# Performance work log

Hardware: AMD Instinct MI355X
Metric: run time of the kernel (lower is better)

## Reference

```python
import jax, jax.numpy as jnp
import numpy as np


def setup_inputs() -> dict:
    key = jax.random.key(0)
    k1, k2 = jax.random.split(key)
    x1 = jax.random.normal(k1, (8192, 256), dtype=jnp.float32)
    x2 = jax.random.normal(k2, (8192, 256), dtype=jnp.float32)
    return {"x1": x1, "x2": x2}


def reference(x1, x2):
    # Euclidean distance matrix, equivalent to torch.cdist(x1, x2, p=2.0).
    # GEMM-based expansion: ||a-b||^2 = ||a||^2 + ||b||^2 - 2 a.b
    sq1 = jnp.sum(x1 * x1, axis=-1, keepdims=True)          # [N, 1]
    sq2 = jnp.sum(x2 * x2, axis=-1, keepdims=True)          # [M, 1]
    cross = jnp.einsum('nd,md->nm', x1, x2)                 # [N, M]
    d2 = sq1 + sq2.T - 2.0 * cross
    d2 = jnp.maximum(d2, 0.0)  # guard tiny negatives from cancellation
    return jnp.sqrt(d2)
```

## Files before the change

### kernel.cpp

```cpp
#include <hip/hip_runtime.h>


typedef __bf16 v8bf __attribute__((ext_vector_type(8)));
typedef float v4f __attribute__((ext_vector_type(4)));

#define NROWS 8192
#define KDIM  256
#define TILE  128
#define BK    64

typedef const __attribute__((address_space(1))) ushort* gas_ushort_p;
typedef __attribute__((address_space(3))) ushort* las_ushort_p;

__device__ __forceinline__ void async_load16(const ushort* g, ushort* l) {
    __builtin_amdgcn_global_load_lds((gas_ushort_p)g, (las_ushort_p)l, 16, 0, 0);
}

__device__ __forceinline__ ushort f2bf_rne(float f) {
    union { float f; unsigned u; } a; a.f = f;
    unsigned u = a.u + 0x7fffu + ((a.u >> 16) & 1u);
    return (ushort)(u >> 16);
}

__global__ __launch_bounds__(256) void cvt_norm_kernel(
    const float* __restrict__ x, ushort* __restrict__ xb, float* __restrict__ sq) {
    const int wave = threadIdx.x >> 6;
    const int lane = threadIdx.x & 63;
    const int row  = blockIdx.x * 4 + wave;
    const float4 v = ((const float4*)(x + (size_t)row * KDIM))[lane];
    float s = v.x * v.x + v.y * v.y + v.z * v.z + v.w * v.w;
#pragma unroll
    for (int off = 32; off; off >>= 1) s += __shfl_down(s, off);
    if (lane == 0) sq[row] = s;
    ushort4 o;
    o.x = f2bf_rne(v.x); o.y = f2bf_rne(v.y);
    o.z = f2bf_rne(v.z); o.w = f2bf_rne(v.w);
    ((ushort4*)(xb + (size_t)row * KDIM))[lane] = o;
}

__global__ __launch_bounds__(256) void cdist_mfma_kernel(
    const ushort* __restrict__ A,
    const ushort* __restrict__ B,
    const float* __restrict__ sq1,
    const float* __restrict__ sq2,
    float* __restrict__ out) {
    __shared__ ushort As[TILE * BK];
    __shared__ ushort Bs[TILE * BK];

    const int bm = blockIdx.x, bn = blockIdx.y;
    const int tid  = threadIdx.x;
    const int wave = tid >> 6;
    const int lane = tid & 63;
    const int wr = wave >> 1;
    const int wc = wave & 1;

    const int lrow = lane >> 3;
    const int lk   = (lane & 7) * 8;

    v4f acc[4][4];
#pragma unroll
    for (int i = 0; i < 4; ++i)
#pragma unroll
        for (int j = 0; j < 4; ++j) acc[i][j] = (v4f){0.f, 0.f, 0.f, 0.f};

    const int half = lane >> 4;
    const int mrow = lane & 15;

    for (int kt = 0; kt < KDIM; kt += BK) {
        __syncthreads();
#pragma unroll
        for (int c = 0; c < 4; ++c) {
            const int rbase = wave * 32 + c * 8;
            const ushort* ga =
                A + (size_t)(bm * TILE + rbase + lrow) * KDIM + kt + lk;
            const ushort* gb =
                B + (size_t)(bn * TILE + rbase + lrow) * KDIM + kt + lk;
            async_load16(ga, &As[rbase * BK]);
            async_load16(gb, &Bs[rbase * BK]);
        }
        __syncthreads();
#pragma unroll
        for (int kk = 0; kk < BK; kk += 32) {
            v8bf a[4], b[4];
#pragma unroll
            for (int i = 0; i < 4; ++i) {
                a[i] = *(const v8bf*)&As[(wr * 64 + i * 16 + mrow) * BK + kk + half * 8];
                b[i] = *(const v8bf*)&Bs[(wc * 64 + i * 16 + mrow) * BK + kk + half * 8];
            }
#pragma unroll
            for (int i = 0; i < 4; ++i)
#pragma unroll
                for (int j = 0; j < 4; ++j)
                    acc[i][j] = __builtin_amdgcn_mfma_f32_16x16x32_bf16(
                        a[i], b[j], acc[i][j], 0, 0, 0);
        }
    }

    const int m0 = bm * TILE + wr * 64;
    const int n0 = bn * TILE + wc * 64;
#pragma unroll
    for (int j = 0; j < 4; ++j) {
        const int col = n0 + j * 16 + mrow;
        const float s2 = sq2[col];
#pragma unroll
        for (int i = 0; i < 4; ++i) {
#pragma unroll
            for (int r = 0; r < 4; ++r) {
                const int row = m0 + i * 16 + half * 4 + r;
                const float d2 = sq1[row] + s2 - 2.0f * acc[i][j][r];
                out[(size_t)row * NROWS + col] = sqrtf(fmaxf(d2, 0.0f));
            }
        }
    }
}

extern "C" void kernel_launch(void* const* d_in, const int* in_sizes, int n_in,
                              void* d_out, int out_size, void* d_ws, size_t ws_size,
                              hipStream_t stream) {
    const float* x1 = (const float*)d_in[0];
    const float* x2 = (const float*)d_in[1];
    float* out = (float*)d_out;

    ushort* Ab = (ushort*)d_ws;
    ushort* Bb = Ab + (size_t)NROWS * KDIM;
    float* sq1 = (float*)(Bb + (size_t)NROWS * KDIM);
    float* sq2 = sq1 + NROWS;

    cvt_norm_kernel<<<NROWS / 4, 256, 0, stream>>>(x1, Ab, sq1);
    cvt_norm_kernel<<<NROWS / 4, 256, 0, stream>>>(x2, Bb, sq2);

    dim3 grid(NROWS / TILE, NROWS / TILE);
    cdist_mfma_kernel<<<grid, 256, 0, stream>>>(Ab, Bb, sq1, sq2, out);
}
```

Measured before the change: 355.0 us.

## Drop LDS staging for register-direct double-buffered loads with XCD-aware tile mapping

The GEMM kernel no longer stages tiles through shared memory with barriers. Each wave now loads its MFMA operands straight from global memory into registers, double-buffering across the eight k-steps. Blocks are remapped so that tiles sharing rows or columns land on the same XCD, which improves L2 reuse. Output uses nontemporal stores, and the two conversion launches are merged into one. The risks are redundant global loads across waves in place of shared LDS reuse, and higher register pressure.

Measured after the change: 382.3 us. +7.7%, slower.

```diff
diff --git a/kernel.cpp b/kernel.cpp
--- a/kernel.cpp
+++ b/kernel.cpp
@@ -6,15 +6,6 @@
 
 #define NROWS 8192
 #define KDIM  256
-#define TILE  128
-#define BK    64
-
-typedef const __attribute__((address_space(1))) ushort* gas_ushort_p;
-typedef __attribute__((address_space(3))) ushort* las_ushort_p;
-
-__device__ __forceinline__ void async_load16(const ushort* g, ushort* l) {
-    __builtin_amdgcn_global_load_lds((gas_ushort_p)g, (las_ushort_p)l, 16, 0, 0);
-}
 
 __device__ __forceinline__ ushort f2bf_rne(float f) {
     union { float f; unsigned u; } a; a.f = f;
@@ -23,10 +14,18 @@
 }
 
 __global__ __launch_bounds__(256) void cvt_norm_kernel(
-    const float* __restrict__ x, ushort* __restrict__ xb, float* __restrict__ sq) {
+    const float* __restrict__ x1, const float* __restrict__ x2,
+    ushort* __restrict__ xb1, ushort* __restrict__ xb2,
+    float* __restrict__ sq1, float* __restrict__ sq2) {
+    const int half2 = NROWS / 4;
+    const float* x = (blockIdx.x < half2) ? x1 : x2;
+    ushort* xb     = (blockIdx.x < half2) ? xb1 : xb2;
+    float* sq      = (blockIdx.x < half2) ? sq1 : sq2;
+    const int bb   = (blockIdx.x < half2) ? blockIdx.x : blockIdx.x - half2;
+
     const int wave = threadIdx.x >> 6;
     const int lane = threadIdx.x & 63;
-    const int row  = blockIdx.x * 4 + wave;
+    const int row  = bb * 4 + wave;
     const float4 v = ((const float4*)(x + (size_t)row * KDIM))[lane];
     float s = v.x * v.x + v.y * v.y + v.z * v.z + v.w * v.w;
 #pragma unroll
@@ -38,24 +37,34 @@
     ((ushort4*)(xb + (size_t)row * KDIM))[lane] = o;
 }
 
-__global__ __launch_bounds__(256) void cdist_mfma_kernel(
+__global__ __launch_bounds__(256) void cdist_nobar_kernel(
     const ushort* __restrict__ A,
     const ushort* __restrict__ B,
     const float* __restrict__ sq1,
     const float* __restrict__ sq2,
     float* __restrict__ out) {
-    __shared__ ushort As[TILE * BK];
-    __shared__ ushort Bs[TILE * BK];
+    const int bid = blockIdx.x;
+    const int xcd = bid & 7;
+    const int cc  = bid >> 3;
+    const int bm  = ((xcd & 3) << 4) | (cc & 15);
+    const int bn  = ((xcd >> 2) << 5) | (cc >> 4);
 
-    const int bm = blockIdx.x, bn = blockIdx.y;
-    const int tid  = threadIdx.x;
-    const int wave = tid >> 6;
-    const int lane = tid & 63;
-    const int wr = wave >> 1;
-    const int wc = wave & 1;
+    const int wave = threadIdx.x >> 6;
+    const int lane = threadIdx.x & 63;
+    const int wr = wave >> 1, wc = wave & 1;
+    const int mrow = lane & 15;
+    const int half = lane >> 4;
 
-    const int lrow = lane >> 3;
-    const int lk   = (lane & 7) * 8;
+    const int m0 = bm * 128 + wr * 64;
+    const int n0 = bn * 128 + wc * 64;
+
+    const ushort* Ap[4];
+    const ushort* Bp[4];
+#pragma unroll
+    for (int i = 0; i < 4; ++i) {
+        Ap[i] = A + (size_t)(m0 + i * 16 + mrow) * KDIM + half * 8;
+        Bp[i] = B + (size_t)(n0 + i * 16 + mrow) * KDIM + half * 8;
+    }
 
     v4f acc[4][4];
 #pragma unroll
@@ -63,52 +72,46 @@
 #pragma unroll
         for (int j = 0; j < 4; ++j) acc[i][j] = (v4f){0.f, 0.f, 0.f, 0.f};
 
-    const int half = lane >> 4;
-    const int mrow = lane & 15;
-
-    for (int kt = 0; kt < KDIM; kt += BK) {
-        __syncthreads();
+    v8bf a[2][4], b[2][4];
 #pragma unroll
-        for (int c = 0; c < 4; ++c) {
-            const int rbase = wave * 32 + c * 8;
-            const ushort* ga =
-                A + (size_t)(bm * TILE + rbase + lrow) * KDIM + kt + lk;
-            const ushort* gb =
-                B + (size_t)(bn * TILE + rbase + lrow) * KDIM + kt + lk;
-            async_load16(ga, &As[rbase * BK]);
-            async_load16(gb, &Bs[rbase * BK]);
-        }
-        __syncthreads();
+    for (int i = 0; i < 4; ++i) {
+        a[0][i] = *(const v8bf*)Ap[i];
+        b[0][i] = *(const v8bf*)Bp[i];
+    }
 #pragma unroll
-        for (int kk = 0; kk < BK; kk += 32) {
-            v8bf a[4], b[4];
+    for (int t = 0; t < 8; ++t) {
+        const int cur = t & 1, nxt = cur ^ 1;
+        if (t < 7) {
 #pragma unroll
             for (int i = 0; i < 4; ++i) {
-                a[i] = *(const v8bf*)&As[(wr * 64 + i * 16 + mrow) * BK + kk + half * 8];
-                b[i] = *(const v8bf*)&Bs[(wc * 64 + i * 16 + mrow) * BK + kk + half * 8];
+                a[nxt][i] = *(const v8bf*)(Ap[i] + (t + 1) * 32);
+                b[nxt][i] = *(const v8bf*)(Bp[i] + (t + 1) * 32);
             }
+        }
 #pragma unroll
-            for (int i = 0; i < 4; ++i)
+        for (int i = 0; i < 4; ++i)
 #pragma unroll
-                for (int j = 0; j < 4; ++j)
-                    acc[i][j] = __builtin_amdgcn_mfma_f32_16x16x32_bf16(
-                        a[i], b[j], acc[i][j], 0, 0, 0);
-        }
+            for (int j = 0; j < 4; ++j)
+                acc[i][j] = __builtin_amdgcn_mfma_f32_16x16x32_bf16(
+                    a[cur][i], b[cur][j], acc[i][j], 0, 0, 0);
     }
 
-    const int m0 = bm * TILE + wr * 64;
-    const int n0 = bn * TILE + wc * 64;
+    float s2v[4];
 #pragma unroll
-    for (int j = 0; j < 4; ++j) {
-        const int col = n0 + j * 16 + mrow;
-        const float s2 = sq2[col];
+    for (int j = 0; j < 4; ++j) s2v[j] = sq2[n0 + j * 16 + mrow];
 #pragma unroll
-        for (int i = 0; i < 4; ++i) {
+    for (int i = 0; i < 4; ++i) {
+        const int rbase = m0 + i * 16 + half * 4;
+        float s1v[4];
 #pragma unroll
-            for (int r = 0; r < 4; ++r) {
-                const int row = m0 + i * 16 + half * 4 + r;
-                const float d2 = sq1[row] + s2 - 2.0f * acc[i][j][r];
-                out[(size_t)row * NROWS + col] = sqrtf(fmaxf(d2, 0.0f));
+        for (int r = 0; r < 4; ++r) s1v[r] = sq1[rbase + r];
+#pragma unroll
+        for (int r = 0; r < 4; ++r) {
+            float* op = out + (size_t)(rbase + r) * NROWS + n0 + mrow;
+#pragma unroll
+            for (int j = 0; j < 4; ++j) {
+                const float d2 = s1v[r] + s2v[j] - 2.0f * acc[i][j][r];
+                __builtin_nontemporal_store(sqrtf(fmaxf(d2, 0.0f)), op + j * 16);
             }
         }
     }
@@ -126,9 +129,7 @@
     float* sq1 = (float*)(Bb + (size_t)NROWS * KDIM);
     float* sq2 = sq1 + NROWS;
 
-    cvt_norm_kernel<<<NROWS / 4, 256, 0, stream>>>(x1, Ab, sq1);
-    cvt_norm_kernel<<<NROWS / 4, 256, 0, stream>>>(x2, Bb, sq2);
+    cvt_norm_kernel<<<NROWS / 2, 256, 0, stream>>>(x1, x2, Ab, Bb, sq1, sq2);
 
-    dim3 grid(NROWS / TILE, NROWS / TILE);
-    cdist_mfma_kernel<<<grid, 256, 0, stream>>>(Ab, Bb, sq1, sq2, out);
+    cdist_nobar_kernel<<<4096, 256, 0, stream>>>(Ab, Bb, sq1, sq2, out);
 }
```
